# Performance work log

Measured on AMD Instinct MI355X. Metric: run time of the kernel, lower is better.

The kernel has to match this reference:

```python
import jax, jax.numpy as jnp
import numpy as np

EPS = 1e-5

def sage_layer(x, src, dst, n_tgt, Wl, bl, Wr, gamma, beta):
    # mean aggregation of source features over incoming edges per target
    msg = x[src]                                         # [E, C] irregular gather
    s = jax.ops.segment_sum(msg, dst, num_segments=n_tgt)
    cnt = jax.ops.segment_sum(jnp.ones((src.shape[0],), x.dtype), dst, num_segments=n_tgt)
    aggr = s / jnp.maximum(cnt, 1.0)[:, None]
    x_tgt = x[:n_tgt]
    h = aggr @ Wl.T + bl + x_tgt @ Wr.T                  # SAGEConv: lin_l(aggr)+lin_r(root)
    h = jax.nn.relu(h)
    mu = jnp.mean(h, axis=0)
    var = jnp.mean((h - mu) ** 2, axis=0)                # biased var (torch BN training)
    return gamma * (h - mu) * jax.lax.rsqrt(var + EPS) + beta

def setup_inputs() -> dict:
    key = jax.random.key(0)
    ks = jax.random.split(key, 16)
    C = 256
    N0, N1, N2 = 200000, 50000, 12500
    E0, E1 = 800000, 400000
    sc = 1.0 / np.sqrt(C)
    return {
        "x": jax.random.normal(ks[0], (N0, C), jnp.float32),
        "ei0_src": jax.random.randint(ks[1], (E0,), 0, N0),
        "ei0_dst": jax.random.randint(ks[2], (E0,), 0, N1),
        "ei1_src": jax.random.randint(ks[3], (E1,), 0, N1),
        "ei1_dst": jax.random.randint(ks[4], (E1,), 0, N2),
        "Wl0": jax.random.normal(ks[5], (C, C), jnp.float32) * sc,
        "bl0": jnp.zeros((C,), jnp.float32),
        "Wr0": jax.random.normal(ks[6], (C, C), jnp.float32) * sc,
        "g0": jnp.ones((C,), jnp.float32),
        "be0": jnp.zeros((C,), jnp.float32),
        "Wl1": jax.random.normal(ks[7], (C, C), jnp.float32) * sc,
        "bl1": jnp.zeros((C,), jnp.float32),
        "Wr1": jax.random.normal(ks[8], (C, C), jnp.float32) * sc,
        "g1": jnp.ones((C,), jnp.float32),
        "be1": jnp.zeros((C,), jnp.float32),
    }

def reference(x, ei0_src, ei0_dst, ei1_src, ei1_dst,
              Wl0, bl0, Wr0, g0, be0, Wl1, bl1, Wr1, g1, be1):
    N1, N2 = 50000, 12500
    x = sage_layer(x, ei0_src, ei0_dst, N1, Wl0, bl0, Wr0, g0, be0)
    x = sage_layer(x, ei1_src, ei1_dst, N2, Wl1, bl1, Wr1, g1, be1)
    return x
```

## Files before the change

kernel.cpp:

```cpp
#include <hip/hip_runtime.h>
#include <cstddef>
#include <cstdint>

#define C 256

typedef __attribute__((ext_vector_type(8))) short short8;
typedef __attribute__((ext_vector_type(4))) float f32x4;

__device__ __forceinline__ ushort f2bf(float f) {
    uint32_t u = __float_as_uint(f);
    u += 0x7FFF + ((u >> 16) & 1);
    return (ushort)(u >> 16);
}
__device__ __forceinline__ float bf2f(ushort u) {
    return __uint_as_float(((uint32_t)u) << 16);
}
__device__ __forceinline__ uint2 pack4(float a, float b, float c, float d) {
    uint2 o;
    o.x = (uint32_t)f2bf(a) | ((uint32_t)f2bf(b) << 16);
    o.y = (uint32_t)f2bf(c) | ((uint32_t)f2bf(d) << 16);
    return o;
}
__device__ __forceinline__ void acc8(uint4 v, float* a) {
    a[0] += bf2f((ushort)(v.x & 0xffff)); a[1] += bf2f((ushort)(v.x >> 16));
    a[2] += bf2f((ushort)(v.y & 0xffff)); a[3] += bf2f((ushort)(v.y >> 16));
    a[4] += bf2f((ushort)(v.z & 0xffff)); a[5] += bf2f((ushort)(v.z >> 16));
    a[6] += bf2f((ushort)(v.w & 0xffff)); a[7] += bf2f((ushort)(v.w >> 16));
}

__global__ __launch_bounds__(256) void prep_kernel(
        const float4* __restrict__ x, int nx4, uint2* __restrict__ xbf,
        const float4* __restrict__ wl0f, const float4* __restrict__ wr0f,
        uint2* __restrict__ wl0b, uint2* __restrict__ wr0b,
        const int* __restrict__ e0d, int* __restrict__ cnt0, int E0,
        const int* __restrict__ e1d, int* __restrict__ cnt1, int E1) {
    const int stride = gridDim.x * blockDim.x;
    int i = blockIdx.x * blockDim.x + threadIdx.x;
    const int sec = blockIdx.y;
    if (sec == 0) {
        for (; i < nx4; i += stride) {
            float4 v = x[i];
            xbf[i] = pack4(v.x, v.y, v.z, v.w);
        }
    } else if (sec == 1) {
        const int nw4 = C * C / 4;
        for (; i < 2 * nw4; i += stride) {
            if (i < nw4) { float4 v = wl0f[i]; wl0b[i] = pack4(v.x, v.y, v.z, v.w); }
            else { float4 v = wr0f[i - nw4]; wr0b[i - nw4] = pack4(v.x, v.y, v.z, v.w); }
        }
    } else if (sec == 2) {
        for (; i < E0; i += stride) atomicAdd(&cnt0[e0d[i]], 1);
    } else {
        for (; i < E1; i += stride) atomicAdd(&cnt1[e1d[i]], 1);
    }
}

__global__ __launch_bounds__(1024) void scan2_kernel(
        const int* __restrict__ cnt0, int* __restrict__ off0, int n0,
        const int* __restrict__ cnt1, int* __restrict__ off1, int n1) {
    const int* cnt = blockIdx.x ? cnt1 : cnt0;
    int* off = blockIdx.x ? off1 : off0;
    int n = blockIdx.x ? n1 : n0;
    __shared__ int buf[1024];
    int chunk = (n + 1023) >> 10;
    int lo = (int)threadIdx.x * chunk;
    int hi = min(lo + chunk, n);
    int s = 0;
    for (int i = lo; i < hi; ++i) s += cnt[i];
    buf[threadIdx.x] = s;
    __syncthreads();
    int xv = s;
    for (int d = 1; d < 1024; d <<= 1) {
        int t = ((int)threadIdx.x >= d) ? buf[threadIdx.x - d] : 0;
        __syncthreads();
        xv += t;
        buf[threadIdx.x] = xv;
        __syncthreads();
    }
    int run = xv - s;
    for (int i = lo; i < hi; ++i) { off[i] = run; run += cnt[i]; }
}

__global__ void scatter2_kernel(
        const int* __restrict__ s0, const int* __restrict__ d0,
        const int* __restrict__ off0, int* __restrict__ cur0, int* __restrict__ esrc0, int E0,
        const int* __restrict__ s1, const int* __restrict__ d1,
        const int* __restrict__ off1, int* __restrict__ cur1, int* __restrict__ esrc1, int E1) {
    int e = blockIdx.x * blockDim.x + threadIdx.x;
    if (e < E0) {
        int d = d0[e];
        esrc0[off0[d] + atomicAdd(&cur0[d], 1)] = s0[e];
    } else if (e < E0 + E1) {
        int i = e - E0;
        int d = d1[i];
        esrc1[off1[d] + atomicAdd(&cur1[d], 1)] = s1[i];
    }
}

__global__ __launch_bounds__(256) void aggregate_kernel(const uint4* __restrict__ xb4,
        const int* __restrict__ esrc, const int* __restrict__ off,
        const int* __restrict__ cnt, uint4* __restrict__ out4, int n_tgt) {
    const int lane = threadIdx.x & 63;
    const int half = lane >> 5, l31 = lane & 31;
    const int t = blockIdx.x * 4 + (threadIdx.x >> 6);
    if (t >= n_tgt) return;
    const int deg = cnt[t];
    const int base = off[t];
    float a[8] = {0.f, 0.f, 0.f, 0.f, 0.f, 0.f, 0.f, 0.f};
    const int deg2 = deg & ~1;
    for (int i = 0; i < deg2; i += 2) {
        int s = esrc[base + i + half];
        uint4 v = xb4[(size_t)s * 32 + l31];
        acc8(v, a);
    }
    if ((deg & 1) && half == 0) {
        int s = esrc[base + deg - 1];
        uint4 v = xb4[(size_t)s * 32 + l31];
        acc8(v, a);
    }
#pragma unroll
    for (int j = 0; j < 8; ++j) a[j] += __shfl_xor(a[j], 32, 64);
    if (half == 0) {
        float inv = 1.0f / (float)(deg > 1 ? deg : 1);
        uint4 o;
        o.x = (uint32_t)f2bf(a[0] * inv) | ((uint32_t)f2bf(a[1] * inv) << 16);
        o.y = (uint32_t)f2bf(a[2] * inv) | ((uint32_t)f2bf(a[3] * inv) << 16);
        o.z = (uint32_t)f2bf(a[4] * inv) | ((uint32_t)f2bf(a[5] * inv) << 16);
        o.w = (uint32_t)f2bf(a[6] * inv) | ((uint32_t)f2bf(a[7] * inv) << 16);
        out4[(size_t)t * 32 + l31] = o;
    }
}

__global__ __launch_bounds__(256) void aggregate_f32_kernel(const float4* __restrict__ x4,
        const int* __restrict__ esrc, const int* __restrict__ off,
        const int* __restrict__ cnt, uint2* __restrict__ aggr, int n_tgt) {
    int w = threadIdx.x >> 6;
    int lane = threadIdx.x & 63;
    int t = blockIdx.x * 4 + w;
    if (t >= n_tgt) return;
    int deg = cnt[t];
    int base = off[t];
    float4 acc = make_float4(0.f, 0.f, 0.f, 0.f);
    for (int i = 0; i < deg; ++i) {
        int s = esrc[base + i];
        float4 v = x4[(size_t)s * 64 + lane];
        acc.x += v.x; acc.y += v.y; acc.z += v.z; acc.w += v.w;
    }
    float inv = 1.0f / (float)(deg > 1 ? deg : 1);
    aggr[(size_t)t * 64 + lane] = pack4(acc.x * inv, acc.y * inv, acc.z * inv, acc.w * inv);
}

#define TM 128
#define TN 128
#define LDK 40

__global__ __launch_bounds__(256) void gemm_bn_mfma(
        const ushort* __restrict__ Aagg, const ushort* __restrict__ Axt,
        const ushort* __restrict__ Wl,  const ushort* __restrict__ Wr,
        const float* __restrict__ bias,
        ushort* __restrict__ h, float* __restrict__ colsum, float* __restrict__ colsq,
        int M) {
    __shared__ ushort As[TM * LDK];
    __shared__ ushort Bs[TN * LDK];
    __shared__ float csum[TN];
    __shared__ float csq[TN];

    const int tid = threadIdx.x;
    const int m0 = blockIdx.y * TM;
    const int n0 = blockIdx.x * TN;
    const int wid = tid >> 6, lane = tid & 63;
    const int l15 = lane & 15, quad = lane >> 4;
    const int wm = (wid & 1) * 64, wn = (wid >> 1) * 64;

    if (tid < TN) { csum[tid] = 0.f; csq[tid] = 0.f; }

    const int srow = tid >> 2;
    const int skoff = (tid & 3) * 8;

    f32x4 acc[4][4];
#pragma unroll
    for (int i = 0; i < 4; ++i)
#pragma unroll
        for (int j = 0; j < 4; ++j) acc[i][j] = (f32x4){0.f, 0.f, 0.f, 0.f};

#pragma unroll 1
    for (int kt = 0; kt < 16; ++kt) {
        const int ks = kt * 32;
        const ushort* Ab = (ks < 256) ? Aagg : Axt;
        const ushort* Bb = (ks < 256) ? Wl : Wr;
        const int k0 = ks & 255;
        int r0 = min(m0 + srow, M - 1);
        int r1 = min(m0 + srow + 64, M - 1);
        uint4 a0 = *(const uint4*)&Ab[(size_t)r0 * C + k0 + skoff];
        uint4 a1 = *(const uint4*)&Ab[(size_t)r1 * C + k0 + skoff];
        uint4 b0 = *(const uint4*)&Bb[(size_t)(n0 + srow) * C + k0 + skoff];
        uint4 b1 = *(const uint4*)&Bb[(size_t)(n0 + srow + 64) * C + k0 + skoff];
        __syncthreads();
        *(uint4*)&As[srow * LDK + skoff] = a0;
        *(uint4*)&As[(srow + 64) * LDK + skoff] = a1;
        *(uint4*)&Bs[srow * LDK + skoff] = b0;
        *(uint4*)&Bs[(srow + 64) * LDK + skoff] = b1;
        __syncthreads();

        short8 af[4], bw[4];
#pragma unroll
        for (int mi = 0; mi < 4; ++mi)
            af[mi] = *(const short8*)&As[(wm + mi * 16 + l15) * LDK + quad * 8];
#pragma unroll
        for (int ni = 0; ni < 4; ++ni)
            bw[ni] = *(const short8*)&Bs[(wn + ni * 16 + l15) * LDK + quad * 8];
#pragma unroll
        for (int mi = 0; mi < 4; ++mi)
#pragma unroll
            for (int ni = 0; ni < 4; ++ni)
                acc[mi][ni] = __builtin_amdgcn_mfma_f32_16x16x32_bf16(
                    af[mi], bw[ni], acc[mi][ni], 0, 0, 0);
    }

    float lsum[4] = {0.f, 0.f, 0.f, 0.f};
    float lsq[4]  = {0.f, 0.f, 0.f, 0.f};
#pragma unroll
    for (int ni = 0; ni < 4; ++ni) {
        const int col = wn + ni * 16 + l15;
        const float bv = bias[n0 + col];
#pragma unroll
        for (int mi = 0; mi < 4; ++mi) {
#pragma unroll
            for (int r = 0; r < 4; ++r) {
                int m = m0 + wm + mi * 16 + quad * 4 + r;
                float v = acc[mi][ni][r] + bv;
                v = fmaxf(v, 0.f);
                if (m < M) {
                    h[(size_t)m * C + n0 + col] = f2bf(v);
                    lsum[ni] += v;
                    lsq[ni] += v * v;
                }
            }
        }
    }
#pragma unroll
    for (int ni = 0; ni < 4; ++ni) {
        const int col = wn + ni * 16 + l15;
        atomicAdd(&csum[col], lsum[ni]);
        atomicAdd(&csq[col], lsq[ni]);
    }
    __syncthreads();
    if (tid < TN) {
        atomicAdd(&colsum[n0 + tid], csum[tid]);
        atomicAdd(&colsq[n0 + tid], csq[tid]);
    }
}

__global__ __launch_bounds__(256) void fixup_kernel(
        const float* __restrict__ colsum, const float* __restrict__ colsq, float invN,
        const float* __restrict__ g0, const float* __restrict__ be0,
        const float* __restrict__ Wl1, const float* __restrict__ Wr1,
        const float* __restrict__ bl1,
        ushort* __restrict__ wl1b, ushort* __restrict__ wr1b, float* __restrict__ bias1) {
    __shared__ float ss[C], st[C];
    __shared__ float red[256];
    const int k = threadIdx.x;
    {
        float m = colsum[k] * invN;
        float v = colsq[k] * invN - m * m;
        float r = rsqrtf(fmaxf(v, 0.f) + 1e-5f);
        float s = g0[k] * r;
        ss[k] = s;
        st[k] = be0[k] - m * s;
    }
    __syncthreads();
    const int n = blockIdx.x;
    float wl = Wl1[(size_t)n * C + k];
    float wr = Wr1[(size_t)n * C + k];
    wl1b[(size_t)n * C + k] = f2bf(wl * ss[k]);
    wr1b[(size_t)n * C + k] = f2bf(wr * ss[k]);
    red[k] = st[k] * (wl + wr);
    __syncthreads();
    for (int d = 128; d > 0; d >>= 1) {
        if (k < d) red[k] += red[k + d];
        __syncthreads();
    }
    if (k == 0) bias1[n] = bl1[n] + red[0];
}

__global__ __launch_bounds__(256) void norm1_kernel(const uint2* __restrict__ hin,
        const float* __restrict__ colsum, const float* __restrict__ colsq, float invN,
        const float* __restrict__ gamma, const float* __restrict__ beta,
        float4* __restrict__ outp, int n4) {
    __shared__ float smu[C], srs[C];
    {
        int k = threadIdx.x;
        float m = colsum[k] * invN;
        float v = colsq[k] * invN - m * m;
        smu[k] = m;
        srs[k] = rsqrtf(fmaxf(v, 0.f) + 1e-5f);
    }
    __syncthreads();
    int i = blockIdx.x * blockDim.x + threadIdx.x;
    if (i >= n4) return;
    int c = (i & 63) << 2;
    uint2 v = hin[i];
    float4 o;
    o.x = gamma[c + 0] * (bf2f((ushort)(v.x & 0xffff)) - smu[c + 0]) * srs[c + 0] + beta[c + 0];
    o.y = gamma[c + 1] * (bf2f((ushort)(v.x >> 16))    - smu[c + 1]) * srs[c + 1] + beta[c + 1];
    o.z = gamma[c + 2] * (bf2f((ushort)(v.y & 0xffff)) - smu[c + 2]) * srs[c + 2] + beta[c + 2];
    o.w = gamma[c + 3] * (bf2f((ushort)(v.y >> 16))    - smu[c + 3]) * srs[c + 3] + beta[c + 3];
    outp[i] = o;
}

extern "C" void kernel_launch(void* const* d_in, const int* in_sizes, int n_in,
                              void* d_out, int out_size, void* d_ws, size_t ws_size,
                              hipStream_t stream) {
    const float* x   = (const float*)d_in[0];
    const int* e0s   = (const int*)d_in[1];
    const int* e0d   = (const int*)d_in[2];
    const int* e1s   = (const int*)d_in[3];
    const int* e1d   = (const int*)d_in[4];
    const float* Wl0 = (const float*)d_in[5];
    const float* bl0 = (const float*)d_in[6];
    const float* Wr0 = (const float*)d_in[7];
    const float* ga0 = (const float*)d_in[8];
    const float* be0 = (const float*)d_in[9];
    const float* Wl1 = (const float*)d_in[10];
    const float* bl1 = (const float*)d_in[11];
    const float* Wr1 = (const float*)d_in[12];
    const float* ga1 = (const float*)d_in[13];
    const float* be1 = (const float*)d_in[14];

    const int N0 = 200000, N1 = 50000, N2 = 12500;
    const int E0 = in_sizes[1];
    const int E1 = in_sizes[3];

    char* ws = (char*)d_ws;
    size_t o = 0;
    auto alloc = [&](size_t bytes) -> char* {
        char* p = ws + o;
        o += (bytes + 255) & ~(size_t)255;
        return p;
    };

    const size_t common =
        (size_t)N1 * C * 2 * 2  + (size_t)E0 * 4 + (size_t)E1 * 4 +
        3 * (size_t)N1 * 4 + 3 * (size_t)N2 * 4 + 8 * C * 4 + 4 * (size_t)C * C * 2 +
        C * 4 + 65536;
    const bool full = ws_size >= common + (size_t)N0 * C * 2;

    ushort* x_bf  = (ushort*)alloc((full ? (size_t)N0 : (size_t)N1) * C * 2);
    ushort* aggr0 = (ushort*)alloc((size_t)N1 * C * 2);
    ushort* h0raw = (ushort*)alloc((size_t)N1 * C * 2);
    ushort* aggr1 = aggr0;
    ushort* h1raw = aggr0 + (size_t)N2 * C;
    int* esrc0 = (int*)alloc((size_t)E0 * sizeof(int));
    int* esrc1 = (int*)alloc((size_t)E1 * sizeof(int));
    int* cnt0 = (int*)alloc(2 * (size_t)N1 * sizeof(int)); int* cur0 = cnt0 + N1;
    int* off0 = (int*)alloc((size_t)N1 * sizeof(int));
    int* cnt1 = (int*)alloc(2 * (size_t)N2 * sizeof(int)); int* cur1 = cnt1 + N2;
    int* off1 = (int*)alloc((size_t)N2 * sizeof(int));
    float* stats = (float*)alloc(8 * C * sizeof(float));
    float* colsum0 = stats,         *colsq0 = stats + C;
    float* colsum1 = stats + 4 * C, *colsq1 = stats + 5 * C;
    ushort* wbf = (ushort*)alloc(4 * (size_t)C * C * 2);
    ushort* wl0b = wbf, *wr0b = wbf + C * C, *wl1b = wbf + 2 * C * C, *wr1b = wbf + 3 * C * C;
    float* bias1 = (float*)alloc(C * sizeof(float));

    hipMemsetAsync(cnt0, 0, 2 * (size_t)N1 * sizeof(int), stream);
    hipMemsetAsync(cnt1, 0, 2 * (size_t)N2 * sizeof(int), stream);
    hipMemsetAsync(stats, 0, 8 * C * sizeof(float), stream);

    {
        int nx4 = (full ? N0 : N1) * C / 4;
        dim3 g(2048, 4);
        prep_kernel<<<g, 256, 0, stream>>>((const float4*)x, nx4, (uint2*)x_bf,
                                           (const float4*)Wl0, (const float4*)Wr0,
                                           (uint2*)wl0b, (uint2*)wr0b,
                                           e0d, cnt0, E0, e1d, cnt1, E1);
    }
    scan2_kernel<<<2, 1024, 0, stream>>>(cnt0, off0, N1, cnt1, off1, N2);
    scatter2_kernel<<<(E0 + E1 + 255) / 256, 256, 0, stream>>>(
        e0s, e0d, off0, cur0, esrc0, E0, e1s, e1d, off1, cur1, esrc1, E1);

    if (full)
        aggregate_kernel<<<N1 / 4, 256, 0, stream>>>((const uint4*)x_bf, esrc0, off0, cnt0,
                                                     (uint4*)aggr0, N1);
    else
        aggregate_f32_kernel<<<N1 / 4, 256, 0, stream>>>((const float4*)x, esrc0, off0, cnt0,
                                                         (uint2*)aggr0, N1);
    dim3 grid0(C / TN, (N1 + TM - 1) / TM);
    gemm_bn_mfma<<<grid0, 256, 0, stream>>>(aggr0, x_bf, wl0b, wr0b, bl0,
                                            h0raw, colsum0, colsq0, N1);
    fixup_kernel<<<C, 256, 0, stream>>>(colsum0, colsq0, 1.0f / (float)N1,
                                        ga0, be0, Wl1, Wr1, bl1, wl1b, wr1b, bias1);

    aggregate_kernel<<<N2 / 4, 256, 0, stream>>>((const uint4*)h0raw, esrc1, off1, cnt1,
                                                 (uint4*)aggr1, N2);
    dim3 grid1(C / TN, (N2 + TM - 1) / TM);
    gemm_bn_mfma<<<grid1, 256, 0, stream>>>(aggr1, h0raw, wl1b, wr1b, bias1,
                                            h1raw, colsum1, colsq1, N2);
    int n4_1 = N2 * C / 4;
    norm1_kernel<<<(n4_1 + 255) / 256, 256, 0, stream>>>((const uint2*)h1raw,
                                                         colsum1, colsq1, 1.0f / (float)N2,
                                                         ga1, be1, (float4*)d_out, n4_1);
}
```

Measured before the change: 707.6 us.

## Widen prep casts, merge memsets, derive degree from CSR offsets, unroll gather

The prep kernel now uses a flat 1-D grid with per-section block counts and casts 8 floats per thread into 16-byte bf16 stores. The separate cursor array is removed: scatter decrements the count array in place and degree is taken from off[t+1]-off[t], which allows one merged memset. The aggregation loop is unrolled to issue two gathers per half-wave in flight. The intent is fewer launches and memsets, wider memory transactions and more memory-level parallelism in the gather, at the cost of a more complex block partition.

New measurement: 686.1 us. 3.0% less time.

```diff
diff --git a/kernel.cpp b/kernel.cpp
--- a/kernel.cpp
+++ b/kernel.cpp
@@ -21,6 +21,14 @@
     o.y = (uint32_t)f2bf(c) | ((uint32_t)f2bf(d) << 16);
     return o;
 }
+__device__ __forceinline__ uint4 pack8(float4 a, float4 b) {
+    uint4 o;
+    o.x = (uint32_t)f2bf(a.x) | ((uint32_t)f2bf(a.y) << 16);
+    o.y = (uint32_t)f2bf(a.z) | ((uint32_t)f2bf(a.w) << 16);
+    o.z = (uint32_t)f2bf(b.x) | ((uint32_t)f2bf(b.y) << 16);
+    o.w = (uint32_t)f2bf(b.z) | ((uint32_t)f2bf(b.w) << 16);
+    return o;
+}
 __device__ __forceinline__ void acc8(uint4 v, float* a) {
     a[0] += bf2f((ushort)(v.x & 0xffff)); a[1] += bf2f((ushort)(v.x >> 16));
     a[2] += bf2f((ushort)(v.y & 0xffff)); a[3] += bf2f((ushort)(v.y >> 16));
@@ -28,30 +36,46 @@
     a[6] += bf2f((ushort)(v.w & 0xffff)); a[7] += bf2f((ushort)(v.w >> 16));
 }
 
+#define PB_CAST 6400
+#define PB_W    64
+#define PB_H0   1024
+#define PB_H1   512
+
 __global__ __launch_bounds__(256) void prep_kernel(
-        const float4* __restrict__ x, int nx4, uint2* __restrict__ xbf,
+        const float4* __restrict__ x4, int nx8, uint4* __restrict__ xbf4,
         const float4* __restrict__ wl0f, const float4* __restrict__ wr0f,
-        uint2* __restrict__ wl0b, uint2* __restrict__ wr0b,
+        uint4* __restrict__ wl0b, uint4* __restrict__ wr0b,
         const int* __restrict__ e0d, int* __restrict__ cnt0, int E0,
         const int* __restrict__ e1d, int* __restrict__ cnt1, int E1) {
-    const int stride = gridDim.x * blockDim.x;
-    int i = blockIdx.x * blockDim.x + threadIdx.x;
-    const int sec = blockIdx.y;
-    if (sec == 0) {
-        for (; i < nx4; i += stride) {
-            float4 v = x[i];
-            xbf[i] = pack4(v.x, v.y, v.z, v.w);
+    const int b = blockIdx.x;
+    if (b < PB_CAST) {
+        const int stride = PB_CAST * 256;
+        for (int i = b * 256 + threadIdx.x; i < nx8; i += stride) {
+            float4 lo = x4[2 * (size_t)i];
+            float4 hi = x4[2 * (size_t)i + 1];
+            xbf4[i] = pack8(lo, hi);
         }
-    } else if (sec == 1) {
-        const int nw4 = C * C / 4;
-        for (; i < 2 * nw4; i += stride) {
-            if (i < nw4) { float4 v = wl0f[i]; wl0b[i] = pack4(v.x, v.y, v.z, v.w); }
-            else { float4 v = wr0f[i - nw4]; wr0b[i - nw4] = pack4(v.x, v.y, v.z, v.w); }
+    } else if (b < PB_CAST + PB_W) {
+        const int nw8 = C * C / 8;
+        const int stride = PB_W * 256;
+        for (int i = (b - PB_CAST) * 256 + threadIdx.x; i < 2 * nw8; i += stride) {
+            if (i < nw8) {
+                float4 lo = wl0f[2 * i], hi = wl0f[2 * i + 1];
+                wl0b[i] = pack8(lo, hi);
+            } else {
+                int j = i - nw8;
+                float4 lo = wr0f[2 * j], hi = wr0f[2 * j + 1];
+                wr0b[j] = pack8(lo, hi);
+            }
         }
-    } else if (sec == 2) {
-        for (; i < E0; i += stride) atomicAdd(&cnt0[e0d[i]], 1);
+    } else if (b < PB_CAST + PB_W + PB_H0) {
+        const int stride = PB_H0 * 256;
+        for (int i = (b - PB_CAST - PB_W) * 256 + threadIdx.x; i < E0; i += stride)
+            atomicAdd(&cnt0[e0d[i]], 1);
     } else {
-        for (; i < E1; i += stride) atomicAdd(&cnt1[e1d[i]], 1);
+        const int stride = PB_H1 * 256;
+        for (int i = (b - PB_CAST - PB_W - PB_H0) * 256 + threadIdx.x; i < E1; i += stride)
+            atomicAdd(&cnt1[e1d[i]], 1);
     }
 }
 
@@ -79,36 +103,47 @@
     }
     int run = xv - s;
     for (int i = lo; i < hi; ++i) { off[i] = run; run += cnt[i]; }
+    if (lo < n && hi == n) off[n] = run;
 }
 
 __global__ void scatter2_kernel(
         const int* __restrict__ s0, const int* __restrict__ d0,
-        const int* __restrict__ off0, int* __restrict__ cur0, int* __restrict__ esrc0, int E0,
+        const int* __restrict__ off0, int* __restrict__ cnt0, int* __restrict__ esrc0, int E0,
         const int* __restrict__ s1, const int* __restrict__ d1,
-        const int* __restrict__ off1, int* __restrict__ cur1, int* __restrict__ esrc1, int E1) {
+        const int* __restrict__ off1, int* __restrict__ cnt1, int* __restrict__ esrc1, int E1) {
     int e = blockIdx.x * blockDim.x + threadIdx.x;
     if (e < E0) {
         int d = d0[e];
-        esrc0[off0[d] + atomicAdd(&cur0[d], 1)] = s0[e];
+        int old = atomicSub(&cnt0[d], 1);
+        esrc0[off0[d] + old - 1] = s0[e];
     } else if (e < E0 + E1) {
         int i = e - E0;
         int d = d1[i];
-        esrc1[off1[d] + atomicAdd(&cur1[d], 1)] = s1[i];
+        int old = atomicSub(&cnt1[d], 1);
+        esrc1[off1[d] + old - 1] = s1[i];
     }
 }
 
 __global__ __launch_bounds__(256) void aggregate_kernel(const uint4* __restrict__ xb4,
         const int* __restrict__ esrc, const int* __restrict__ off,
-        const int* __restrict__ cnt, uint4* __restrict__ out4, int n_tgt) {
+        uint4* __restrict__ out4, int n_tgt) {
     const int lane = threadIdx.x & 63;
     const int half = lane >> 5, l31 = lane & 31;
     const int t = blockIdx.x * 4 + (threadIdx.x >> 6);
     if (t >= n_tgt) return;
-    const int deg = cnt[t];
     const int base = off[t];
+    const int deg = off[t + 1] - base;
     float a[8] = {0.f, 0.f, 0.f, 0.f, 0.f, 0.f, 0.f, 0.f};
-    const int deg2 = deg & ~1;
-    for (int i = 0; i < deg2; i += 2) {
+    int i = 0;
+    for (; i + 4 <= deg; i += 4) {
+        int s0 = esrc[base + i + half];
+        int s1 = esrc[base + i + 2 + half];
+        uint4 v0 = xb4[(size_t)s0 * 32 + l31];
+        uint4 v1 = xb4[(size_t)s1 * 32 + l31];
+        acc8(v0, a);
+        acc8(v1, a);
+    }
+    for (; i + 2 <= deg; i += 2) {
         int s = esrc[base + i + half];
         uint4 v = xb4[(size_t)s * 32 + l31];
         acc8(v, a);
@@ -133,13 +168,13 @@
 
 __global__ __launch_bounds__(256) void aggregate_f32_kernel(const float4* __restrict__ x4,
         const int* __restrict__ esrc, const int* __restrict__ off,
-        const int* __restrict__ cnt, uint2* __restrict__ aggr, int n_tgt) {
+        uint2* __restrict__ aggr, int n_tgt) {
     int w = threadIdx.x >> 6;
     int lane = threadIdx.x & 63;
     int t = blockIdx.x * 4 + w;
     if (t >= n_tgt) return;
-    int deg = cnt[t];
     int base = off[t];
+    int deg = off[t + 1] - base;
     float4 acc = make_float4(0.f, 0.f, 0.f, 0.f);
     for (int i = 0; i < deg; ++i) {
         int s = esrc[base + i];
@@ -340,11 +375,20 @@
     };
 
     const size_t common =
-        (size_t)N1 * C * 2 * 2  + (size_t)E0 * 4 + (size_t)E1 * 4 +
-        3 * (size_t)N1 * 4 + 3 * (size_t)N2 * 4 + 8 * C * 4 + 4 * (size_t)C * C * 2 +
-        C * 4 + 65536;
+        (size_t)N1 * C * 2 * 2 + (size_t)E0 * 4 + (size_t)E1 * 4 +
+        ((size_t)N1 + N2 + 8 * C) * 4 + ((size_t)N1 + N2 + 2) * 4 +
+        4 * (size_t)C * C * 2 + C * 4 + 65536;
     const bool full = ws_size >= common + (size_t)N0 * C * 2;
 
+    int* cnt0 = (int*)alloc(((size_t)N1 + N2 + 8 * C) * sizeof(int));
+    int* cnt1 = cnt0 + N1;
+    float* stats = (float*)(cnt1 + N2);
+    float* colsum0 = stats,         *colsq0 = stats + C;
+    float* colsum1 = stats + 4 * C, *colsq1 = stats + 5 * C;
+    const size_t zbytes = ((size_t)N1 + N2 + 8 * C) * sizeof(int);
+
+    int* off0 = (int*)alloc(((size_t)N1 + 1) * sizeof(int));
+    int* off1 = (int*)alloc(((size_t)N2 + 1) * sizeof(int));
     ushort* x_bf  = (ushort*)alloc((full ? (size_t)N0 : (size_t)N1) * C * 2);
     ushort* aggr0 = (ushort*)alloc((size_t)N1 * C * 2);
     ushort* h0raw = (ushort*)alloc((size_t)N1 * C * 2);
@@ -352,38 +396,28 @@
     ushort* h1raw = aggr0 + (size_t)N2 * C;
     int* esrc0 = (int*)alloc((size_t)E0 * sizeof(int));
     int* esrc1 = (int*)alloc((size_t)E1 * sizeof(int));
-    int* cnt0 = (int*)alloc(2 * (size_t)N1 * sizeof(int)); int* cur0 = cnt0 + N1;
-    int* off0 = (int*)alloc((size_t)N1 * sizeof(int));
-    int* cnt1 = (int*)alloc(2 * (size_t)N2 * sizeof(int)); int* cur1 = cnt1 + N2;
-    int* off1 = (int*)alloc((size_t)N2 * sizeof(int));
-    float* stats = (float*)alloc(8 * C * sizeof(float));
-    float* colsum0 = stats,         *colsq0 = stats + C;
-    float* colsum1 = stats + 4 * C, *colsq1 = stats + 5 * C;
     ushort* wbf = (ushort*)alloc(4 * (size_t)C * C * 2);
     ushort* wl0b = wbf, *wr0b = wbf + C * C, *wl1b = wbf + 2 * C * C, *wr1b = wbf + 3 * C * C;
     float* bias1 = (float*)alloc(C * sizeof(float));
 
-    hipMemsetAsync(cnt0, 0, 2 * (size_t)N1 * sizeof(int), stream);
-    hipMemsetAsync(cnt1, 0, 2 * (size_t)N2 * sizeof(int), stream);
-    hipMemsetAsync(stats, 0, 8 * C * sizeof(float), stream);
+    hipMemsetAsync(cnt0, 0, zbytes, stream);
 
     {
-        int nx4 = (full ? N0 : N1) * C / 4;
-        dim3 g(2048, 4);
-        prep_kernel<<<g, 256, 0, stream>>>((const float4*)x, nx4, (uint2*)x_bf,
-                                           (const float4*)Wl0, (const float4*)Wr0,
-                                           (uint2*)wl0b, (uint2*)wr0b,
-                                           e0d, cnt0, E0, e1d, cnt1, E1);
+        int nx8 = (full ? N0 : N1) * C / 8;
+        prep_kernel<<<PB_CAST + PB_W + PB_H0 + PB_H1, 256, 0, stream>>>(
+            (const float4*)x, nx8, (uint4*)x_bf,
+            (const float4*)Wl0, (const float4*)Wr0, (uint4*)wl0b, (uint4*)wr0b,
+            e0d, cnt0, E0, e1d, cnt1, E1);
     }
     scan2_kernel<<<2, 1024, 0, stream>>>(cnt0, off0, N1, cnt1, off1, N2);
     scatter2_kernel<<<(E0 + E1 + 255) / 256, 256, 0, stream>>>(
-        e0s, e0d, off0, cur0, esrc0, E0, e1s, e1d, off1, cur1, esrc1, E1);
+        e0s, e0d, off0, cnt0, esrc0, E0, e1s, e1d, off1, cnt1, esrc1, E1);
 
     if (full)
-        aggregate_kernel<<<N1 / 4, 256, 0, stream>>>((const uint4*)x_bf, esrc0, off0, cnt0,
+        aggregate_kernel<<<N1 / 4, 256, 0, stream>>>((const uint4*)x_bf, esrc0, off0,
                                                      (uint4*)aggr0, N1);
     else
-        aggregate_f32_kernel<<<N1 / 4, 256, 0, stream>>>((const float4*)x, esrc0, off0, cnt0,
+        aggregate_f32_kernel<<<N1 / 4, 256, 0, stream>>>((const float4*)x, esrc0, off0,
                                                          (uint2*)aggr0, N1);
     dim3 grid0(C / TN, (N1 + TM - 1) / TM);
     gemm_bn_mfma<<<grid0, 256, 0, stream>>>(aggr0, x_bf, wl0b, wr0b, bl0,
@@ -391,7 +425,7 @@
     fixup_kernel<<<C, 256, 0, stream>>>(colsum0, colsq0, 1.0f / (float)N1,
                                         ga0, be0, Wl1, Wr1, bl1, wl1b, wr1b, bias1);
 
-    aggregate_kernel<<<N2 / 4, 256, 0, stream>>>((const uint4*)h0raw, esrc1, off1, cnt1,
+    aggregate_kernel<<<N2 / 4, 256, 0, stream>>>((const uint4*)h0raw, esrc1, off1,
                                                  (uint4*)aggr1, N2);
     dim3 grid1(C / TN, (N2 + TM - 1) / TM);
     gemm_bn_mfma<<<grid1, 256, 0, stream>>>(aggr1, h0raw, wl1b, wr1b, bias1,
```
